# Performance work log

Measured on AMD Instinct MI355X. Metric: run time of the kernel, lower is better.

The kernel has to match this reference:

```python
import jax, jax.numpy as jnp
import numpy as np
from jax import lax

B, L, D, H, NW, NL = 4, 256, 768, 384, 4, 9
WINDOWS = (3, 5, 7, 9)


def setup_inputs() -> dict:
    key = jax.random.key(0)
    ks = jax.random.split(key, 12)
    s = 0.05
    return {
        "seq_out": jax.random.normal(ks[0], (B, L, D), jnp.float32),
        "valid_ids": jax.random.randint(ks[1], (B, L), 0, 2),
        "w_ih_f": jax.random.normal(ks[2], (NW, 4 * H, D), jnp.float32) * s,
        "w_hh_f": jax.random.normal(ks[3], (NW, 4 * H, H), jnp.float32) * s,
        "b_ih_f": jax.random.normal(ks[4], (NW, 4 * H), jnp.float32) * s,
        "b_hh_f": jax.random.normal(ks[5], (NW, 4 * H), jnp.float32) * s,
        "w_ih_b": jax.random.normal(ks[6], (NW, 4 * H, D), jnp.float32) * s,
        "w_hh_b": jax.random.normal(ks[7], (NW, 4 * H, H), jnp.float32) * s,
        "b_ih_b": jax.random.normal(ks[8], (NW, 4 * H), jnp.float32) * s,
        "b_hh_b": jax.random.normal(ks[9], (NW, 4 * H), jnp.float32) * s,
        "lin_w": jax.random.normal(ks[10], (NL, D), jnp.float32) * s,
        "lin_b": jnp.zeros((NL,), jnp.float32),
    }


def _lstm_last(win, mask, W_ih, W_hh, b, reverse):
    # invalid (out-of-range) steps leave the state untouched, so the final
    # carry equals the hidden state after the last valid step (PyTorch LSTM math).
    Bx, Lx, w, Dx = win.shape
    Hh = W_hh.shape[1]

    def step(carry, xm):
        h, c = carry
        x_t, m = xm  # [B,L,D], [L]
        gates = x_t @ W_ih.T + h @ W_hh.T + b  # [B,L,4H], gate order i,f,g,o
        i, f, g, o = jnp.split(gates, 4, axis=-1)
        i = jax.nn.sigmoid(i)
        f = jax.nn.sigmoid(f)
        g = jnp.tanh(g)
        o = jax.nn.sigmoid(o)
        c_new = f * c + i * g
        h_new = o * jnp.tanh(c_new)
        m3 = m[None, :, None]
        return (jnp.where(m3, h_new, h), jnp.where(m3, c_new, c)), None

    init = (jnp.zeros((Bx, Lx, Hh), win.dtype), jnp.zeros((Bx, Lx, Hh), win.dtype))
    (h, _), _ = lax.scan(step, init, (jnp.moveaxis(win, 2, 0), mask.T), reverse=reverse)
    return h


def _window_features(x, w, Wif, Whf, bf, Wib, Whb, bb):
    # Faithful vectorization of windows_sequence: the sorted index_list for
    # position i is the contiguous slice [max(0,i-w//2) .. min(L-1,i+w//2)].
    Bx, Lx, Dx = x.shape
    half = w // 2
    pos = jnp.arange(Lx)[:, None] + jnp.arange(-half, half + 1)[None, :]  # [L,w]
    mask = (pos >= 0) & (pos < Lx)
    idx = jnp.clip(pos, 0, Lx - 1)
    win = x[:, idx, :]  # [B,L,w,D]
    h_f = _lstm_last(win, mask, Wif, Whf, bf, reverse=False)  # fwd dir: last output
    h_b = _lstm_last(win, mask, Wib, Whb, bb, reverse=True)   # bwd dir over reversed window
    return jnp.concatenate([h_f, h_b], axis=-1)  # [B,L,D]


def _valid_scatter(x, valid_ids):
    # Left-pack tokens with valid_ids==1 (the nested Python scatter loop).
    Bx, Lx, Dx = x.shape
    v = valid_ids.astype(jnp.int32)
    dest = jnp.where(v == 1, jnp.cumsum(v, axis=1) - 1, Lx)  # invalid -> pad slot

    def pack(row_x, row_d):
        return jnp.zeros((Lx + 1, Dx), row_x.dtype).at[row_d].set(row_x)[:Lx]

    return jax.vmap(pack)(x, dest)


def reference(seq_out, valid_ids, w_ih_f, w_hh_f, b_ih_f, b_hh_f,
              w_ih_b, w_hh_b, b_ih_b, b_hh_b, lin_w, lin_b):
    x = _valid_scatter(seq_out, valid_ids)  # [B,L,D]; dropout is identity in eval
    locals_ = [
        _window_features(x, WINDOWS[i],
                         w_ih_f[i], w_hh_f[i], b_ih_f[i] + b_hh_f[i],
                         w_ih_b[i], w_hh_b[i], b_ih_b[i] + b_hh_b[i])
        for i in range(NW)
    ]
    muti = jnp.stack(locals_, axis=2)  # [B,L,NW,D]
    # dot-att: query is the (packed) sequence output itself
    attn = jax.nn.softmax(
        jnp.einsum('bld,blwd->blw', x, muti) / jnp.sqrt(jnp.float32(D)), axis=-1)
    local_feat = jnp.einsum('blw,blwd->bld', attn, muti)
    out = x + local_feat
    return out @ lin_w.T + lin_b  # logits [B,L,NL]
```

## Files before the change

kernel.cpp:

```cpp
#include <hip/hip_runtime.h>
#include <math.h>

#define LL 256
#define DD 768
#define HH 384
#define G4 1536
#define NWIN 4
#define NLIN 9
#define NPOS 1024
#define PROJ_N 12288
#define HSTRIDE 520

typedef __attribute__((ext_vector_type(8))) short short8;
typedef __attribute__((ext_vector_type(4))) short short4v;
typedef __attribute__((ext_vector_type(16))) float f32x16;

static __device__ __forceinline__ float bf2f(unsigned short u) {
    union { unsigned int i; float f; } v; v.i = ((unsigned int)u) << 16; return v.f;
}
static __device__ __forceinline__ unsigned short f2bf(float f) {
    unsigned int u = __float_as_uint(f);
    u += 0x7fff + ((u >> 16) & 1);
    return (unsigned short)(u >> 16);
}
static __device__ __forceinline__ float fsig(float x) {
    return __builtin_amdgcn_rcpf(1.f + __expf(-x));
}
static __device__ __forceinline__ float ftanh(float x) {
    return 1.f - 2.f * __builtin_amdgcn_rcpf(1.f + __expf(2.f * x));
}

__global__ __launch_bounds__(256) void prep_kernel(
        const float* __restrict__ seq, const int* __restrict__ valid,
        unsigned short* __restrict__ xfrag,
        const float* __restrict__ wihF, const float* __restrict__ wihB,
        unsigned short* __restrict__ wfih,
        const float* __restrict__ whhF, const float* __restrict__ whhB,
        unsigned short* __restrict__ wfhh,
        const float* __restrict__ lin_b, float* __restrict__ out) {
    const int tid = threadIdx.x;
    if (blockIdx.x < 128) {
        const int b = blockIdx.x >> 5;
        const int chunk = blockIdx.x & 31;
        __shared__ int dest[LL];
        __shared__ int wsum[4];
        __shared__ int nvalid;
        const int v = valid[b * LL + tid];
        const unsigned long long m = __ballot(v != 0);
        const int lane = tid & 63, wvi = tid >> 6;
        const int pre = __popcll(m & (((unsigned long long)1 << lane) - 1));
        if (lane == 63) wsum[wvi] = pre + (v ? 1 : 0);
        __syncthreads();
        int base = 0;
#pragma unroll
        for (int k = 0; k < 4; ++k) if (k < wvi) base += wsum[k];
        dest[tid] = v ? (base + pre) : -1;
        if (tid == 0) nvalid = wsum[0] + wsum[1] + wsum[2] + wsum[3];
        __syncthreads();
        const int nv = nvalid;
        for (int l = chunk * 8; l < chunk * 8 + 8; ++l) {
            const int d = dest[l];
            if (d >= 0) {
                const float* src = seq + (size_t)(b * LL + l) * DD;
                const int pos = b * LL + d;
                const int pt = pos >> 5, pl = pos & 31;
                for (int j = tid; j < DD / 8; j += 256) {
                    const float4 v0 = ((const float4*)src)[2 * j];
                    const float4 v1 = ((const float4*)src)[2 * j + 1];
                    short8 pv;
                    pv[0] = (short)f2bf(v0.x); pv[1] = (short)f2bf(v0.y);
                    pv[2] = (short)f2bf(v0.z); pv[3] = (short)f2bf(v0.w);
                    pv[4] = (short)f2bf(v1.x); pv[5] = (short)f2bf(v1.y);
                    pv[6] = (short)f2bf(v1.z); pv[7] = (short)f2bf(v1.w);
                    *(short8*)(xfrag + ((size_t)(pt * 48 + (j >> 1)) * 512 + (pl + 32 * (j & 1)) * 8)) = pv;
                }
            }
            if (l >= nv) {
                const int pos = b * LL + l;
                const int pt = pos >> 5, pl = pos & 31;
                const short8 zv = {};
                for (int j = tid; j < DD / 8; j += 256)
                    *(short8*)(xfrag + ((size_t)(pt * 48 + (j >> 1)) * 512 + (pl + 32 * (j & 1)) * 8)) = zv;
            }
        }
    } else if (blockIdx.x < 896) {
        __shared__ unsigned short lds[32 * 768];
        const int cb = blockIdx.x - 128;
        const int isIH = cb < 384;
        const int vblk = isIH ? cb : (cb - 384);
        const int K = isIH ? DD : HH;
        const float* srcF = isIH ? wihF : whhF;
        const float* srcB = isIH ? wihB : whhB;
        unsigned short* dst = isIH ? wfih : wfhh;
        const int vrow0 = vblk * 32;
        const int chain = vrow0 / G4;
        const int dir = chain >> 2, wi = chain & 3;
        const float* src = (dir ? srcB : srcF) + (size_t)(wi * G4 + (vrow0 % G4)) * K;
        const int total = 32 * K;
        for (int i = tid * 4; i < total; i += 1024) {
            const float4 v = *(const float4*)(src + i);
            lds[i + 0] = f2bf(v.x); lds[i + 1] = f2bf(v.y);
            lds[i + 2] = f2bf(v.z); lds[i + 3] = f2bf(v.w);
        }
        __syncthreads();
        const int nks = K >> 4;
        for (int slot = tid; slot < nks * 64; slot += 256) {
            const int ks = slot >> 6;
            const int lane = slot & 63;
            const int row = lane & 31;
            const int kb = ks * 16 + (lane >> 5) * 8;
            const short8 v = *(const short8*)&lds[row * K + kb];
            *(short8*)(dst + ((size_t)vblk * nks + ks) * 512 + lane * 8) = v;
        }
    } else {
        for (int i = tid; i < NPOS * NLIN; i += 256)
            out[i] = lin_b[i % NLIN];
    }
}

__global__ __launch_bounds__(256) void proj_mfma(
        const unsigned short* __restrict__ xf,
        const unsigned short* __restrict__ wf,
        const float* __restrict__ bihf, const float* __restrict__ bhhf,
        const float* __restrict__ bihb, const float* __restrict__ bhhb,
        unsigned short* __restrict__ proj) {
    __shared__ __align__(16) unsigned short st[4 * 4096];
    const int wv = threadIdx.x >> 6;
    const int lane = threadIdx.x & 63;
    const int colid = lane & 31, hq = lane >> 5;
    const int chain = blockIdx.x & 7;
    const int r8 = blockIdx.x >> 3;
    const int us = r8 % 12;
    const int mtg = r8 / 12;
    const int dir = chain >> 2, wi = chain & 3;

    const unsigned short* bP = wf + (size_t)((chain * 48 + wv * 12 + us) * 48) * 512 + lane * 8;
    const unsigned short* aP = xf + (size_t)(mtg * 4 * 48) * 512 + lane * 8;

    f32x16 acc[4] = {};
#pragma unroll 4
    for (int ks = 0; ks < 48; ++ks) {
        const short8 bv = *(const short8*)(bP + ks * 512);
        const short8 a0 = *(const short8*)(aP + (0 * 48 + ks) * 512);
        const short8 a1 = *(const short8*)(aP + (1 * 48 + ks) * 512);
        const short8 a2 = *(const short8*)(aP + (2 * 48 + ks) * 512);
        const short8 a3 = *(const short8*)(aP + (3 * 48 + ks) * 512);
        acc[0] = __builtin_amdgcn_mfma_f32_32x32x16_bf16(a0, bv, acc[0], 0, 0, 0);
        acc[1] = __builtin_amdgcn_mfma_f32_32x32x16_bf16(a1, bv, acc[1], 0, 0, 0);
        acc[2] = __builtin_amdgcn_mfma_f32_32x32x16_bf16(a2, bv, acc[2], 0, 0, 0);
        acc[3] = __builtin_amdgcn_mfma_f32_32x32x16_bf16(a3, bv, acc[3], 0, 0, 0);
    }
    const int br = wv * HH + us * 32 + colid;
    const float bv = (dir ? bihb : bihf)[wi * G4 + br] + (dir ? bhhb : bhhf)[wi * G4 + br];
#pragma unroll
    for (int i = 0; i < 4; ++i) {
#pragma unroll
        for (int r = 0; r < 16; ++r) {
            const int row = (r & 3) + 8 * (r >> 2) + 4 * hq;
            st[i * 4096 + (row * 32 + colid) * 4 + wv] = f2bf(acc[i][r] + bv);
        }
    }
    __syncthreads();
#pragma unroll
    for (int j = 0; j < 8; ++j) {
        const int idx = j * 256 + threadIdx.x;
        const int i = idx >> 9, rem = idx & 511;
        const int pl = rem >> 4, q = rem & 15;
        const int pos = (mtg * 4 + i) * 32 + pl;
        *(int4*)(proj + (size_t)pos * PROJ_N + chain * G4 + us * 128 + q * 8) =
            ((const int4*)st)[idx];
    }
}

__global__ __launch_bounds__(768, 3) void lstm_fused(
        const unsigned short* __restrict__ Wf,
        const unsigned short* __restrict__ proj,
        unsigned short* __restrict__ hfin) {
    const int p = blockIdx.x & 3, sub = (blockIdx.x >> 2) & 1;
    const int slot = blockIdx.x >> 3;
    const int chainA[4] = {3, 7, 2, 6};
    const int chainB[4] = {0, 4, 1, 5};
    const int chain = (slot < 16) ? chainA[p] : chainB[p];
    const int pt = sub * 16 + (slot & 15);
    const int dir = chain >> 2, wi = chain & 3;
    const int w = 3 + 2 * wi, half = wi + 1;
    const int tid = threadIdx.x;
    const int lane = tid & 63, wv = tid >> 6;
    const int colid = lane & 31, hq = lane >> 5;
    const int uu = wv * 32 + colid;
    const int m0 = pt * 32, b = m0 >> 8, l0 = m0 & 255;

    __shared__ __align__(16) unsigned short Hbuf[2][24 * HSTRIDE];
    float c[16];
#pragma unroll
    for (int r = 0; r < 16; ++r) c[r] = 0.f;

    const unsigned short* projb = proj + (size_t)(b * LL) * PROJ_N + chain * G4 + uu * 4;
    const unsigned short* Wb = Wf + (size_t)((chain * 48 + wv) * 24) * 512 + lane * 8;
    const int ksp = uu >> 4, khp = (uu >> 3) & 1, jp = uu & 7;
    const int hslot = ksp * HSTRIDE + khp * 256 + jp;

    for (int s = 0; s < w; ++s) {
        const int t = dir ? (w - 1 - s) : s;
        const int tmh = t - half;
        unsigned short* cur = Hbuf[s & 1];
        const unsigned short* prev = Hbuf[(s & 1) ^ 1];

        short4v pj[16];
#pragma unroll
        for (int r = 0; r < 16; ++r) {
            const int row = (r & 3) + 8 * (r >> 2) + 4 * hq;
            int src = l0 + row + tmh;
            src = src < 0 ? 0 : (src > LL - 1 ? LL - 1 : src);
            pj[r] = *(const short4v*)(projb + src * PROJ_N);
        }

        f32x16 acc0 = {}, acc1 = {}, acc2 = {}, acc3 = {};
        if (s > 0) {
            const unsigned short* Alds = prev + lane * 8;
#pragma unroll 4
            for (int ks = 0; ks < 24; ++ks) {
                const short8 av  = *(const short8*)(Alds + ks * HSTRIDE);
                const short8 bv0 = *(const short8*)(Wb + (size_t)(0 * 288 + ks) * 512);
                const short8 bv1 = *(const short8*)(Wb + (size_t)(1 * 288 + ks) * 512);
                const short8 bv2 = *(const short8*)(Wb + (size_t)(2 * 288 + ks) * 512);
                const short8 bv3 = *(const short8*)(Wb + (size_t)(3 * 288 + ks) * 512);
                acc0 = __builtin_amdgcn_mfma_f32_32x32x16_bf16(av, bv0, acc0, 0, 0, 0);
                acc1 = __builtin_amdgcn_mfma_f32_32x32x16_bf16(av, bv1, acc1, 0, 0, 0);
                acc2 = __builtin_amdgcn_mfma_f32_32x32x16_bf16(av, bv2, acc2, 0, 0, 0);
                acc3 = __builtin_amdgcn_mfma_f32_32x32x16_bf16(av, bv3, acc3, 0, 0, 0);
            }
        }

#pragma unroll
        for (int r = 0; r < 16; ++r) {
            const int row = (r & 3) + 8 * (r >> 2) + 4 * hq;
            const int src = l0 + row + tmh;
            unsigned short hv;
            if (src >= 0 && src < LL) {
                const float gi = acc0[r] + bf2f((unsigned short)pj[r][0]);
                const float gf = acc1[r] + bf2f((unsigned short)pj[r][1]);
                const float gg = acc2[r] + bf2f((unsigned short)pj[r][2]);
                const float go = acc3[r] + bf2f((unsigned short)pj[r][3]);
                c[r] = fsig(gf) * c[r] + fsig(gi) * ftanh(gg);
                hv = f2bf(fsig(go) * ftanh(c[r]));
            } else {
                hv = (s == 0) ? (unsigned short)0 : prev[hslot + row * 8];
            }
            cur[hslot + row * 8] = hv;
        }
        __syncthreads();
    }

    const unsigned short* fin = Hbuf[(w - 1) & 1];
    unsigned short* ho = hfin + (size_t)chain * (NPOS * HH) + (size_t)pt * 12288;
#pragma unroll
    for (int i = tid; i < 1536; i += 768) {
        const int ks = i >> 6, off = i & 63;
        *(int4*)(ho + ks * 512 + off * 8) = *(const int4*)(fin + ks * HSTRIDE + off * 8);
    }
}

__global__ __launch_bounds__(192) void attn_scores_kernel(
        const unsigned short* __restrict__ xfrag,
        const unsigned short* __restrict__ hfin,
        float* __restrict__ scores) {
    const int pt = blockIdx.x >> 3, seg = blockIdx.x & 7;
    const int dir = seg >> 2, q = seg & 3;
    const int tid = threadIdx.x;
    const int lane = tid & 63, wv3 = tid >> 6;
    const int pos = lane & 31;
    __shared__ float scp[3][4][32];

    const unsigned short* xb = xfrag + ((size_t)(pt * 48 + 24 * dir)) * 512 + lane * 8;
    const unsigned short* hb0 = hfin + (size_t)(dir * 4) * (NPOS * HH) + (size_t)pt * 12288 + lane * 8;

    float sc4[4] = {0.f, 0.f, 0.f, 0.f};
#pragma unroll
    for (int k = 0; k < 2; ++k) {
        const int ks = q * 6 + wv3 * 2 + k;
        const short8 xv = *(const short8*)(xb + ks * 512);
        float xf[8];
#pragma unroll
        for (int j = 0; j < 8; ++j) xf[j] = bf2f((unsigned short)xv[j]);
#pragma unroll
        for (int wi = 0; wi < 4; ++wi) {
            const short8 hv = *(const short8*)(hb0 + (size_t)wi * (NPOS * HH) + ks * 512);
#pragma unroll
            for (int j = 0; j < 8; ++j)
                sc4[wi] = fmaf(xf[j], bf2f((unsigned short)hv[j]), sc4[wi]);
        }
    }
#pragma unroll
    for (int wi = 0; wi < 4; ++wi) sc4[wi] += __shfl_down(sc4[wi], 32);
    if (lane < 32) {
#pragma unroll
        for (int wi = 0; wi < 4; ++wi) scp[wv3][wi][pos] = sc4[wi];
    }
    __syncthreads();
    if (tid < 32) {
#pragma unroll
        for (int wi = 0; wi < 4; ++wi) {
            const float v = scp[0][wi][tid] + scp[1][wi][tid] + scp[2][wi][tid];
            scores[(((size_t)pt * 8 + seg) * 4 + wi) * 32 + tid] = v;
        }
    }
}

__global__ __launch_bounds__(192) void attn_out2_kernel(
        const unsigned short* __restrict__ xfrag,
        const unsigned short* __restrict__ hfin,
        const float* __restrict__ scores,
        const float* __restrict__ lin_w,
        float* __restrict__ out) {
    const int pt = blockIdx.x >> 3, seg = blockIdx.x & 7;
    const int dir = seg >> 2, q = seg & 3;
    const int tid = threadIdx.x;
    const int lane = tid & 63, wv3 = tid >> 6;
    const int pos = lane & 31, kh = lane >> 5;
    const float inv_sqrt_d = 0.03608439182435161f;
    __shared__ float redp[3][32][10];

    float s[4];
#pragma unroll
    for (int wi = 0; wi < 4; ++wi) {
        float v = 0.f;
#pragma unroll
        for (int s2 = 0; s2 < 8; ++s2)
            v += scores[(((size_t)pt * 8 + s2) * 4 + wi) * 32 + pos];
        s[wi] = v * inv_sqrt_d;
    }
    float mx = fmaxf(fmaxf(s[0], s[1]), fmaxf(s[2], s[3]));
    float denom = 0.f;
    float aw[4];
#pragma unroll
    for (int wi = 0; wi < 4; ++wi) { aw[wi] = __expf(s[wi] - mx); denom += aw[wi]; }
    const float rd = __builtin_amdgcn_rcpf(denom);
#pragma unroll
    for (int wi = 0; wi < 4; ++wi) aw[wi] *= rd;

    const unsigned short* xb = xfrag + ((size_t)(pt * 48 + 24 * dir)) * 512 + lane * 8;
    const unsigned short* hb0 = hfin + (size_t)(dir * 4) * (NPOS * HH) + (size_t)pt * 12288 + lane * 8;

    float rp[9];
#pragma unroll
    for (int r = 0; r < 9; ++r) rp[r] = 0.f;
#pragma unroll
    for (int k = 0; k < 2; ++k) {
        const int ks = q * 6 + wv3 * 2 + k;
        const short8 xv = *(const short8*)(xb + ks * 512);
        float ov[8];
#pragma unroll
        for (int j = 0; j < 8; ++j) ov[j] = bf2f((unsigned short)xv[j]);
#pragma unroll
        for (int wi = 0; wi < 4; ++wi) {
            const short8 hv = *(const short8*)(hb0 + (size_t)wi * (NPOS * HH) + ks * 512);
#pragma unroll
            for (int j = 0; j < 8; ++j)
                ov[j] = fmaf(aw[wi], bf2f((unsigned short)hv[j]), ov[j]);
        }
        const int dbase = dir * 384 + ks * 16 + kh * 8;
#pragma unroll
        for (int r = 0; r < 9; ++r) {
            const float4 lw0 = *(const float4*)(lin_w + r * DD + dbase);
            const float4 lw1 = *(const float4*)(lin_w + r * DD + dbase + 4);
            rp[r] += ov[0] * lw0.x + ov[1] * lw0.y + ov[2] * lw0.z + ov[3] * lw0.w
                   + ov[4] * lw1.x + ov[5] * lw1.y + ov[6] * lw1.z + ov[7] * lw1.w;
        }
    }
#pragma unroll
    for (int r = 0; r < 9; ++r) rp[r] += __shfl_down(rp[r], 32);
    if (lane < 32) {
#pragma unroll
        for (int r = 0; r < 9; ++r) redp[wv3][pos][r] = rp[r];
    }
    __syncthreads();
    if (tid < 96) {
#pragma unroll
        for (int e = 0; e < 3; ++e) {
            const int flat = tid * 3 + e;
            const int p2 = flat / 9, r = flat % 9;
            const float sum = redp[0][p2][r] + redp[1][p2][r] + redp[2][p2][r];
            atomicAdd(&out[(size_t)(pt * 32 + p2) * NLIN + r], sum);
        }
    }
}

extern "C" void kernel_launch(void* const* d_in, const int* in_sizes, int n_in,
                              void* d_out, int out_size, void* d_ws, size_t ws_size,
                              hipStream_t stream) {
    (void)in_sizes; (void)n_in; (void)out_size; (void)ws_size;
    const float* seq   = (const float*)d_in[0];
    const int*   valid = (const int*)d_in[1];
    const float* wih_f = (const float*)d_in[2];
    const float* whh_f = (const float*)d_in[3];
    const float* bih_f = (const float*)d_in[4];
    const float* bhh_f = (const float*)d_in[5];
    const float* wih_b = (const float*)d_in[6];
    const float* whh_b = (const float*)d_in[7];
    const float* bih_b = (const float*)d_in[8];
    const float* bhh_b = (const float*)d_in[9];
    const float* lin_w = (const float*)d_in[10];
    const float* lin_b = (const float*)d_in[11];
    float* out = (float*)d_out;

    unsigned short* xfrag = (unsigned short*)d_ws;
    unsigned short* proj  = xfrag + (size_t)NPOS * DD;
    unsigned short* wfhh  = proj + (size_t)NPOS * PROJ_N;
    unsigned short* wfih  = wfhh + (size_t)4718592;
    unsigned short* hfin  = wfih + (size_t)9437184;
    float* scores = (float*)(hfin + (size_t)3145728);

    prep_kernel<<<897, 256, 0, stream>>>(seq, valid, xfrag,
                                         wih_f, wih_b, wfih,
                                         whh_f, whh_b, wfhh,
                                         lin_b, out);
    proj_mfma<<<768, 256, 0, stream>>>(xfrag, wfih, bih_f, bhh_f, bih_b, bhh_b, proj);
    lstm_fused<<<256, 768, 0, stream>>>(wfhh, proj, hfin);
    attn_scores_kernel<<<256, 192, 0, stream>>>(xfrag, hfin, scores);
    attn_out2_kernel<<<256, 192, 0, stream>>>(xfrag, hfin, scores, lin_w, out);
}
```

Measured before the change: 277.3 us.

## Stage LSTM input projections in an LDS ring buffer with one-row prefetch

The fused LSTM kernel no longer gathers the 16 projection rows from global memory at every window step. It now preloads 32 rows into a shared-memory ring of 33 slots, then fetches just one new row per step, issued before the recurrent MFMA loop so the load overlaps the matmul. Neighbouring window steps share most of their rows, so this cuts repeated global traffic. The cost is about 100KB of extra LDS per block, which forces occupancy down to one block per CU (launch bounds lowered to 1), and adds a serial 32-row preload before the loop.

```diff
diff --git a/kernel.cpp b/kernel.cpp
--- a/kernel.cpp
+++ b/kernel.cpp
@@ -10,6 +10,7 @@
 #define NPOS 1024
 #define PROJ_N 12288
 #define HSTRIDE 520
+#define PSLOTS 33
 
 typedef __attribute__((ext_vector_type(8))) short short8;
 typedef __attribute__((ext_vector_type(4))) short short4v;
@@ -172,7 +173,7 @@
     }
 }
 
-__global__ __launch_bounds__(768, 3) void lstm_fused(
+__global__ __launch_bounds__(768, 1) void lstm_fused(
         const unsigned short* __restrict__ Wf,
         const unsigned short* __restrict__ proj,
         unsigned short* __restrict__ hfin) {
@@ -191,14 +192,25 @@
     const int m0 = pt * 32, b = m0 >> 8, l0 = m0 & 255;
 
     __shared__ __align__(16) unsigned short Hbuf[2][24 * HSTRIDE];
+    __shared__ __align__(16) unsigned short Pring[PSLOTS][1536];
     float c[16];
 #pragma unroll
     for (int r = 0; r < 16; ++r) c[r] = 0.f;
 
-    const unsigned short* projb = proj + (size_t)(b * LL) * PROJ_N + chain * G4 + uu * 4;
+    const unsigned int* projU = (const unsigned int*)(proj
+        + (size_t)(b * LL) * PROJ_N + chain * G4);
     const unsigned short* Wb = Wf + (size_t)((chain * 48 + wv) * 24) * 512 + lane * 8;
     const int ksp = uu >> 4, khp = (uu >> 3) & 1, jp = uu & 7;
     const int hslot = ksp * HSTRIDE + khp * 256 + jp;
+
+    const int t0 = dir ? (w - 1) : 0;
+    for (int i = 0; i < 32; ++i) {
+        int src = l0 + i + t0 - half;
+        src = src < 0 ? 0 : (src > LL - 1 ? LL - 1 : src);
+        ((unsigned int*)&Pring[src % PSLOTS][0])[tid] =
+            projU[(size_t)src * (PROJ_N / 2) + tid];
+    }
+    __syncthreads();
 
     for (int s = 0; s < w; ++s) {
         const int t = dir ? (w - 1 - s) : s;
@@ -206,13 +218,13 @@
         unsigned short* cur = Hbuf[s & 1];
         const unsigned short* prev = Hbuf[(s & 1) ^ 1];
 
-        short4v pj[16];
-#pragma unroll
-        for (int r = 0; r < 16; ++r) {
-            const int row = (r & 3) + 8 * (r >> 2) + 4 * hq;
-            int src = l0 + row + tmh;
-            src = src < 0 ? 0 : (src > LL - 1 ? LL - 1 : src);
-            pj[r] = *(const short4v*)(projb + src * PROJ_N);
+        int nsrc = -1;
+        unsigned int pref = 0;
+        if (s + 1 < w) {
+            const int tn = dir ? (w - 2 - s) : (s + 1);
+            nsrc = dir ? (l0 + tn - half) : (l0 + 31 + tn - half);
+            nsrc = nsrc < 0 ? 0 : (nsrc > LL - 1 ? LL - 1 : nsrc);
+            pref = projU[(size_t)nsrc * (PROJ_N / 2) + tid];
         }
 
         f32x16 acc0 = {}, acc1 = {}, acc2 = {}, acc3 = {};
@@ -236,12 +248,14 @@
         for (int r = 0; r < 16; ++r) {
             const int row = (r & 3) + 8 * (r >> 2) + 4 * hq;
             const int src = l0 + row + tmh;
+            const int cs = src < 0 ? 0 : (src > LL - 1 ? LL - 1 : src);
             unsigned short hv;
             if (src >= 0 && src < LL) {
-                const float gi = acc0[r] + bf2f((unsigned short)pj[r][0]);
-                const float gf = acc1[r] + bf2f((unsigned short)pj[r][1]);
-                const float gg = acc2[r] + bf2f((unsigned short)pj[r][2]);
-                const float go = acc3[r] + bf2f((unsigned short)pj[r][3]);
+                const short4v pj = *(const short4v*)&Pring[cs % PSLOTS][uu * 4];
+                const float gi = acc0[r] + bf2f((unsigned short)pj[0]);
+                const float gf = acc1[r] + bf2f((unsigned short)pj[1]);
+                const float gg = acc2[r] + bf2f((unsigned short)pj[2]);
+                const float go = acc3[r] + bf2f((unsigned short)pj[3]);
                 c[r] = fsig(gf) * c[r] + fsig(gi) * ftanh(gg);
                 hv = f2bf(fsig(go) * ftanh(c[r]));
             } else {
@@ -249,6 +263,9 @@
             }
             cur[hslot + row * 8] = hv;
         }
+
+        if (nsrc >= 0)
+            ((unsigned int*)&Pring[nsrc % PSLOTS][0])[tid] = pref;
         __syncthreads();
     }
 
```

Result: faster. 267.9 us (-3.4%).
